# Kernel tuning notes

Hardware: AMD Instinct MI355X
Metric: run time of the kernel (lower is better)

Reference implementation:

```python
import jax, jax.numpy as jnp
import numpy as np

D_MODEL, D_INNER, D_STATE, D_CONV, DT_RANK = 2048, 4096, 16, 4, 128
B, T = 2, 1024


def setup_inputs() -> dict:
    key = jax.random.key(0)
    ks = jax.random.split(key, 8)
    dt_init_std = DT_RANK ** -0.5
    # dt bias init per the torch code: inv softplus of dt in [dt_min, dt_max]
    dt = jnp.exp(jax.random.uniform(ks[6], (D_INNER,)) * (np.log(0.1) - np.log(0.001)) + np.log(0.001))
    dt = jnp.clip(dt, 1e-4, None)
    dt_proj_b = dt + jnp.log(-jnp.expm1(-dt))
    A_log = jnp.log(jnp.tile(jnp.arange(1, D_STATE + 1, dtype=jnp.float32)[None, :], (D_INNER, 1)))
    return {
        "x": jax.random.normal(ks[0], (B, T, D_MODEL), jnp.float32),
        "h": jnp.zeros((B, D_INNER, D_STATE), jnp.float32),
        "conv_cache": jnp.zeros((B, D_INNER, D_CONV - 1), jnp.float32),
        "in_proj_w": jax.random.normal(ks[1], (2 * D_INNER, D_MODEL), jnp.float32) * 0.02,
        "conv_w": jax.random.normal(ks[2], (D_INNER, D_CONV), jnp.float32) * (1.0 / np.sqrt(D_CONV)),
        "conv_b": jnp.zeros((D_INNER,), jnp.float32),
        "x_proj_w": jax.random.normal(ks[3], (DT_RANK + 2 * D_STATE, D_INNER), jnp.float32) * 0.02,
        "dt_proj_w": jax.random.uniform(ks[4], (D_INNER, DT_RANK), jnp.float32, -dt_init_std, dt_init_std),
        "dt_proj_b": dt_proj_b,
        "A_log": A_log,
        "D_param": jnp.ones((D_INNER,), jnp.float32),
        "out_proj_w": jax.random.normal(ks[5], (D_MODEL, D_INNER), jnp.float32) * 0.02,
    }


def _forward(x, h, conv_cache, in_proj_w, conv_w, conv_b, x_proj_w,
             dt_proj_w, dt_proj_b, A_log, D_param, out_proj_w):
    Tlen = x.shape[1]
    xz = x @ in_proj_w.T                                  # (B,T,2*d_inner)
    xi, z = jnp.split(xz, 2, axis=-1)
    # causal depthwise conv with cache: concat history then valid conv
    xc = jnp.concatenate([jnp.swapaxes(conv_cache, 1, 2), xi], axis=1)  # (B,T+3,d_inner)
    new_conv_cache = jnp.swapaxes(xc[:, -(D_CONV - 1):, :], 1, 2)       # (B,d_inner,3)
    xconv = sum(xc[:, k:k + Tlen, :] * conv_w[:, k] for k in range(D_CONV)) + conv_b
    xs = jax.nn.silu(xconv)                               # (B,T,d_inner)
    # SSM params per step
    dbc = xs @ x_proj_w.T                                 # (B,T,dt_rank+2n)
    delta, Bm, Cm = jnp.split(dbc, [DT_RANK, DT_RANK + D_STATE], axis=-1)
    delta = jax.nn.softplus(delta @ dt_proj_w.T + dt_proj_b)  # (B,T,d_inner)
    A = -jnp.exp(A_log)                                   # (d_inner,n)
    dA = jnp.exp(jnp.einsum('btd,dn->btdn', delta, A))    # (B,T,d,n)
    dBx = jnp.einsum('btd,btn,btd->btdn', delta, Bm, xs)  # (B,T,d,n)

    def step(hc, inp):
        dA_t, dBx_t, C_t = inp
        hc = dA_t * hc + dBx_t                            # (B,d,n)
        return hc, jnp.einsum('bdn,bn->bd', hc, C_t)

    h_last, ys = jax.lax.scan(
        step, h,
        (jnp.moveaxis(dA, 1, 0), jnp.moveaxis(dBx, 1, 0), jnp.moveaxis(Cm, 1, 0)))
    y = jnp.moveaxis(ys, 0, 1) + D_param * xs             # (B,T,d_inner)
    out = (y * jax.nn.silu(z)) @ out_proj_w.T             # (B,T,d_model)
    return out, h_last, new_conv_cache


def reference(x, h, conv_cache, in_proj_w, conv_w, conv_b, x_proj_w,
              dt_proj_w, dt_proj_b, A_log, D_param, out_proj_w):
    return _forward(x, h, conv_cache, in_proj_w, conv_w, conv_b, x_proj_w,
                    dt_proj_w, dt_proj_b, A_log, D_param, out_proj_w)
```

## Files before the change

kernel.cpp:

```cpp
#include <hip/hip_runtime.h>
#include <hip/hip_bf16.h>
#include <math.h>

#define D_MODEL 2048
#define D_INNER 4096
#define D_STATE 16
#define D_CONV  4
#define DT_RANK 128
#define NB      2
#define TT      1024
#define M_TOT   (NB * TT)
#define NC      16
#define CL      64
#define TC      16

typedef __bf16 bf16x8_t __attribute__((ext_vector_type(8)));
typedef float  f32x4_t  __attribute__((ext_vector_type(4)));

__global__ __launch_bounds__(256) void fused_cast(
    const float* __restrict__ x,  const float* __restrict__ wi,
    const float* __restrict__ wo, const float* __restrict__ wx,
    const float* __restrict__ wdt,
    __bf16* __restrict__ x16,  __bf16* __restrict__ wi16,
    __bf16* __restrict__ wo16, __bf16* __restrict__ wx16,
    __bf16* __restrict__ wdt16, __bf16* __restrict__ dbc16)
{
    const size_t g = (size_t)blockIdx.x * 256 + threadIdx.x;
    const float* src; __bf16* dst; size_t off;
    if      (g < 524288)  { src = x;   dst = x16;   off = g; }
    else if (g < 2621440) { src = wi;  dst = wi16;  off = g - 524288; }
    else if (g < 3670016) { src = wo;  dst = wo16;  off = g - 2621440; }
    else if (g < 3801088) { off = g - 3670016; dst = wx16;
                            src = (g < 3751936) ? wx : nullptr; }
    else if (g < 3866624) { src = wdt; dst = wdt16; off = g - 3801088; }
    else                  { src = nullptr; dst = dbc16; off = g - 3866624; }

    bf16x8_t v;
    if (src) {
        const float4 f0 = ((const float4*)src)[2 * off];
        const float4 f1 = ((const float4*)src)[2 * off + 1];
        v[0] = (__bf16)f0.x; v[1] = (__bf16)f0.y; v[2] = (__bf16)f0.z; v[3] = (__bf16)f0.w;
        v[4] = (__bf16)f1.x; v[5] = (__bf16)f1.y; v[6] = (__bf16)f1.z; v[7] = (__bf16)f1.w;
    } else {
        v = (bf16x8_t)(__bf16)0.f;
    }
    ((bf16x8_t*)dst)[off] = v;
}

__global__ __launch_bounds__(256) void reduce_out(
    const float4* __restrict__ p0, const float4* __restrict__ p1,
    float4* __restrict__ o)
{
    const size_t g = (size_t)blockIdx.x * 256 + threadIdx.x;
    const float4 a = p0[g];
    const float4 b = p1[g];
    o[g] = make_float4(a.x + b.x, a.y + b.y, a.z + b.z, a.w + b.w);
}

__global__ __launch_bounds__(512, 2) void gemm_bf16_256(
    const __bf16* __restrict__ A, int lda,
    const __bf16* __restrict__ W, int ldw,
    __bf16* __restrict__ C, int ldc,
    int nt)
{
    __shared__ __bf16 As[4 * 128 * 64];
    __shared__ __bf16 Bs[4 * 128 * 64];

    const int tid = threadIdx.x;
    const int w   = tid >> 6;
    const int l   = tid & 63;
    const int m0  = blockIdx.y * 256;
    const int n0  = blockIdx.x * 256;
    const int wm  = (w >> 2) * 128;
    const int wn  = (w & 3) * 64;

    const int sl   = ((l & 7) ^ (l >> 3)) & 7;
    const int srow = 2 * (w * 16 + (l >> 3)) + (sl >> 2);
    const int scol = (sl & 3) * 8;
    const __bf16* gA = A + (size_t)(m0 + srow) * lda + scol;
    const __bf16* gB = W + (size_t)(n0 + srow) * ldw + scol;
    __bf16* lA = &As[(size_t)w * 1024];
    __bf16* lB = &Bs[(size_t)w * 1024];

    const int fr  = l & 15;
    const int swz = ((((fr & 1) * 4) + (l >> 4)) ^ ((fr >> 1) & 7)) * 8;
    const int aoff = wm * 32 + (fr >> 1) * 64 + swz;
    const int boff = wn * 32 + (fr >> 1) * 64 + swz;

    f32x4_t acc[8][4] = {};

#define STAGE_A(t, q) { \
    const __bf16* s0_ = gA + (size_t)(t) * 32; \
    __builtin_amdgcn_global_load_lds((const __attribute__((address_space(1))) void*)s0_, \
        (__attribute__((address_space(3))) void*)(lA + (q) * 8192), 16, 0, 0); \
    __builtin_amdgcn_global_load_lds((const __attribute__((address_space(1))) void*)(s0_ + (size_t)16 * lda), \
        (__attribute__((address_space(3))) void*)(lA + (q) * 8192 + 512), 16, 0, 0); }
#define STAGE_B(t, q) { \
    const __bf16* s0_ = gB + (size_t)(t) * 32; \
    __builtin_amdgcn_global_load_lds((const __attribute__((address_space(1))) void*)s0_, \
        (__attribute__((address_space(3))) void*)(lB + (q) * 8192), 16, 0, 0); \
    __builtin_amdgcn_global_load_lds((const __attribute__((address_space(1))) void*)(s0_ + (size_t)16 * ldw), \
        (__attribute__((address_space(3))) void*)(lB + (q) * 8192 + 512), 16, 0, 0); }

    STAGE_A(0, 0); STAGE_B(0, 0);
    STAGE_A(1, 1); STAGE_B(1, 1);
    asm volatile("s_waitcnt vmcnt(4)" ::: "memory");
    __builtin_amdgcn_s_barrier();

    for (int t = 0; t < nt; ++t) {
        const int q  = t & 3;
        const int qn = (t + 2) & 3;
        const __bf16* Aq = &As[q * 8192];
        const __bf16* Bq = &Bs[q * 8192];
        bf16x8_t av[4], bv[4];

#pragma unroll
        for (int i = 0; i < 4; i++)
            av[i] = *(const bf16x8_t*)&Aq[aoff + i * 512];
#pragma unroll
        for (int i = 0; i < 4; i++)
            bv[i] = *(const bf16x8_t*)&Bq[boff + i * 512];
        if (t + 2 < nt) STAGE_A(t + 2, qn);
        __builtin_amdgcn_s_barrier();
        asm volatile("s_waitcnt lgkmcnt(0)" ::: "memory");
        __builtin_amdgcn_sched_barrier(0);
        __builtin_amdgcn_s_setprio(1);
#pragma unroll
        for (int mt = 0; mt < 4; mt++)
#pragma unroll
            for (int nn = 0; nn < 4; nn++)
                acc[mt][nn] = __builtin_amdgcn_mfma_f32_16x16x32_bf16(
                    av[mt], bv[nn], acc[mt][nn], 0, 0, 0);
        __builtin_amdgcn_s_setprio(0);
        __builtin_amdgcn_s_barrier();

#pragma unroll
        for (int i = 0; i < 4; i++)
            av[i] = *(const bf16x8_t*)&Aq[aoff + (i + 4) * 512];
        if (t + 2 < nt) STAGE_B(t + 2, qn);
        __builtin_amdgcn_s_barrier();
        asm volatile("s_waitcnt lgkmcnt(0)" ::: "memory");
        __builtin_amdgcn_sched_barrier(0);
        __builtin_amdgcn_s_setprio(1);
#pragma unroll
        for (int mt = 0; mt < 4; mt++)
#pragma unroll
            for (int nn = 0; nn < 4; nn++)
                acc[mt + 4][nn] = __builtin_amdgcn_mfma_f32_16x16x32_bf16(
                    av[mt], bv[nn], acc[mt + 4][nn], 0, 0, 0);
        __builtin_amdgcn_s_setprio(0);
        if (t + 2 < nt) asm volatile("s_waitcnt vmcnt(4)" ::: "memory");
        else            asm volatile("s_waitcnt vmcnt(0)" ::: "memory");
        __builtin_amdgcn_s_barrier();
    }
#undef STAGE_A
#undef STAGE_B

    const int cn = n0 + wn + fr;
    const int rb = m0 + wm + (l >> 4) * 4;
#pragma unroll
    for (int mt = 0; mt < 8; mt++)
#pragma unroll
        for (int nn = 0; nn < 4; nn++)
#pragma unroll
            for (int r = 0; r < 4; r++)
                C[(size_t)(rb + mt * 16 + r) * ldc + cn + nn * 16] =
                    (__bf16)acc[mt][nn][r];
}

template <int EPI, int KSTEP, typename OutT>
__global__ __launch_bounds__(256) void gemm_bf16_nt(
    const __bf16* __restrict__ A, int lda,
    const __bf16* __restrict__ W, int ldw,
    OutT* __restrict__ C, int ldc,
    int Kloop, int Nmax, const float* __restrict__ bias, size_t czoff)
{
    __shared__ __bf16 As[128 * KSTEP];
    __shared__ __bf16 Bs[128 * KSTEP];

    const int tid  = threadIdx.x;
    const int wave = tid >> 6;
    const int lane = tid & 63;
    const int m0 = blockIdx.y * 128;
    const int n0 = blockIdx.x * 128;
    const int mw = (wave >> 1) * 64;
    const int nw = (wave & 1) * 64;
    const int koff = blockIdx.z * Kloop;
    C += (size_t)blockIdx.z * czoff;

    f32x4_t acc[4][4] = {};

    const int g0 = wave * 2;
    const int rA = g0 * 16 + (lane >> 2);
    const int kk = (lane & 3) * 8;

    const __bf16* gA0 = A + (size_t)(m0 + rA) * lda + kk + koff;
    const __bf16* gA1 = gA0 + (size_t)16 * lda;
    const __bf16* gB0 = W + (size_t)(n0 + rA) * ldw + kk + koff;
    const __bf16* gB1 = gB0 + (size_t)16 * ldw;

    __bf16* lA0 = &As[(size_t)g0 * 512];
    __bf16* lA1 = &As[(size_t)(g0 + 1) * 512];
    __bf16* lB0 = &Bs[(size_t)g0 * 512];
    __bf16* lB1 = &Bs[(size_t)(g0 + 1) * 512];

    const int fr = lane & 15;
    const int fk = (lane >> 4) * 8;

    for (int k0 = 0; k0 < Kloop; k0 += KSTEP) {
#pragma unroll
        for (int p = 0; p < KSTEP / 32; p++) {
            const int kp = k0 + p * 32;
            const int lp = p * 4096;
            __builtin_amdgcn_global_load_lds(
                (const __attribute__((address_space(1))) void*)(gA0 + kp),
                (__attribute__((address_space(3))) void*)(lA0 + lp), 16, 0, 0);
            __builtin_amdgcn_global_load_lds(
                (const __attribute__((address_space(1))) void*)(gA1 + kp),
                (__attribute__((address_space(3))) void*)(lA1 + lp), 16, 0, 0);
            __builtin_amdgcn_global_load_lds(
                (const __attribute__((address_space(1))) void*)(gB0 + kp),
                (__attribute__((address_space(3))) void*)(lB0 + lp), 16, 0, 0);
            __builtin_amdgcn_global_load_lds(
                (const __attribute__((address_space(1))) void*)(gB1 + kp),
                (__attribute__((address_space(3))) void*)(lB1 + lp), 16, 0, 0);
        }
        __syncthreads();

#pragma unroll
        for (int p = 0; p < KSTEP / 32; p++) {
            const int lp = p * 4096;
            bf16x8_t av[4], bv[4];
#pragma unroll
            for (int mt = 0; mt < 4; mt++)
                av[mt] = *(const bf16x8_t*)&As[lp + (mw + mt * 16 + fr) * 32 + fk];
#pragma unroll
            for (int nt = 0; nt < 4; nt++)
                bv[nt] = *(const bf16x8_t*)&Bs[lp + (nw + nt * 16 + fr) * 32 + fk];

#pragma unroll
            for (int mt = 0; mt < 4; mt++)
#pragma unroll
                for (int nt = 0; nt < 4; nt++)
                    acc[mt][nt] = __builtin_amdgcn_mfma_f32_16x16x32_bf16(
                        av[mt], bv[nt], acc[mt][nt], 0, 0, 0);
        }
        __syncthreads();
    }

    const int cn = n0 + nw + (lane & 15);
    const int rb = m0 + mw + (lane >> 4) * 4;
#pragma unroll
    for (int mt = 0; mt < 4; mt++)
#pragma unroll
        for (int nt = 0; nt < 4; nt++) {
            const int n = cn + nt * 16;
            if (n >= Nmax) continue;
#pragma unroll
            for (int r = 0; r < 4; r++) {
                float v = acc[mt][nt][r];
                OutT* p = &C[(size_t)(rb + mt * 16 + r) * ldc + n];
                if (EPI == 1) {
                    v += bias[n];
                    v = (v > 20.f) ? v : __logf(1.f + __expf(v));
                    *p = (OutT)v;
                } else if (EPI == 2) {
                    atomicAdd((float*)p, v);
                } else {
                    *p = (OutT)v;
                }
            }
        }
}

__global__ __launch_bounds__(256) void gemm_dt(
    const float* __restrict__ A,
    const __bf16* __restrict__ W,
    __bf16* __restrict__ C,
    const float* __restrict__ bias)
{
    __shared__ __bf16 As[4 * 64 * 32];
    __shared__ __bf16 Bs[4 * 64 * 32];

    const int tid  = threadIdx.x;
    const int wave = tid >> 6;
    const int lane = tid & 63;
    const int m0 = blockIdx.y * 64;
    const int n0 = blockIdx.x * 64;
    const int mw = (wave >> 1) * 32;
    const int nw = (wave & 1) * 32;

    {
        const int r  = tid >> 2;
        const int cg = (tid & 3) * 8;
        const float* gA = A + (size_t)(m0 + r) * 160 + cg;
#pragma unroll
        for (int p = 0; p < 4; p++) {
            const float4 f0 = *(const float4*)(gA + p * 32);
            const float4 f1 = *(const float4*)(gA + p * 32 + 4);
            bf16x8_t v;
            v[0] = (__bf16)f0.x; v[1] = (__bf16)f0.y; v[2] = (__bf16)f0.z; v[3] = (__bf16)f0.w;
            v[4] = (__bf16)f1.x; v[5] = (__bf16)f1.y; v[6] = (__bf16)f1.z; v[7] = (__bf16)f1.w;
            *(bf16x8_t*)&As[p * 2048 + r * 32 + cg] = v;
        }
    }
    {
        const int rB = wave * 16 + (lane >> 2);
        const int kk = (lane & 3) * 8;
        const __bf16* gB = W + (size_t)(n0 + rB) * 128 + kk;
        __bf16* lB = &Bs[wave * 512];
#pragma unroll
        for (int p = 0; p < 4; p++) {
            __builtin_amdgcn_global_load_lds(
                (const __attribute__((address_space(1))) void*)(gB + p * 32),
                (__attribute__((address_space(3))) void*)(lB + p * 2048), 16, 0, 0);
        }
    }
    __syncthreads();

    const int fr = lane & 15;
    const int fk = (lane >> 4) * 8;
    f32x4_t acc[2][2] = {};
#pragma unroll
    for (int p = 0; p < 4; p++) {
        bf16x8_t av[2], bv[2];
#pragma unroll
        for (int mt = 0; mt < 2; mt++)
            av[mt] = *(const bf16x8_t*)&As[p * 2048 + (mw + mt * 16 + fr) * 32 + fk];
#pragma unroll
        for (int nt = 0; nt < 2; nt++)
            bv[nt] = *(const bf16x8_t*)&Bs[p * 2048 + (nw + nt * 16 + fr) * 32 + fk];
#pragma unroll
        for (int mt = 0; mt < 2; mt++)
#pragma unroll
            for (int nt = 0; nt < 2; nt++)
                acc[mt][nt] = __builtin_amdgcn_mfma_f32_16x16x32_bf16(
                    av[mt], bv[nt], acc[mt][nt], 0, 0, 0);
    }

    const int cn = n0 + nw + (lane & 15);
    const int rb = m0 + mw + (lane >> 4) * 4;
#pragma unroll
    for (int mt = 0; mt < 2; mt++)
#pragma unroll
        for (int nt = 0; nt < 2; nt++) {
            const int n = cn + nt * 16;
            const float bs = bias[n];
#pragma unroll
            for (int r = 0; r < 4; r++) {
                float v = acc[mt][nt][r] + bs;
                v = (v > 20.f) ? v : __logf(1.f + __expf(v));
                C[(size_t)(rb + mt * 16 + r) * 4096 + n] = (__bf16)v;
            }
        }
}

__global__ __launch_bounds__(256) void conv_silu(
    const __bf16* __restrict__ xz16,
    const float* __restrict__ conv_cache,
    const float* __restrict__ conv_w,
    const float* __restrict__ conv_b,
    __bf16* __restrict__ xs16,
    float* __restrict__ cc_out)
{
    const int b  = blockIdx.z;
    const int d  = blockIdx.y * 256 + threadIdx.x;
    const int t0 = blockIdx.x * TC;

    const float4 w  = *(const float4*)&conv_w[d * 4];
    const float bias = conv_b[d];

    float v[TC + 3];
    if (t0 == 0) {
        v[0] = conv_cache[(b * D_INNER + d) * 3 + 0];
        v[1] = conv_cache[(b * D_INNER + d) * 3 + 1];
        v[2] = conv_cache[(b * D_INNER + d) * 3 + 2];
    } else {
        v[0] = (float)xz16[(size_t)(b * TT + t0 - 3) * 8192 + d];
        v[1] = (float)xz16[(size_t)(b * TT + t0 - 2) * 8192 + d];
        v[2] = (float)xz16[(size_t)(b * TT + t0 - 1) * 8192 + d];
    }
#pragma unroll
    for (int k = 0; k < TC; k++)
        v[k + 3] = (float)xz16[(size_t)(b * TT + t0 + k) * 8192 + d];

#pragma unroll
    for (int k = 0; k < TC; k++) {
        float c = v[k] * w.x + v[k + 1] * w.y + v[k + 2] * w.z + v[k + 3] * w.w + bias;
        float s = c / (1.f + __expf(-c));
        xs16[(size_t)(b * TT + t0 + k) * 4096 + d] = (__bf16)s;
    }

    if (t0 + TC == TT) {
        cc_out[(b * D_INNER + d) * 3 + 0] = v[TC];
        cc_out[(b * D_INNER + d) * 3 + 1] = v[TC + 1];
        cc_out[(b * D_INNER + d) * 3 + 2] = v[TC + 2];
    }
}

__global__ __launch_bounds__(256) void scan_phase_a(
    const __bf16* __restrict__ delta16,
    const float* __restrict__ dbc,
    const __bf16* __restrict__ xs16,
    const float* __restrict__ A_log,
    float* __restrict__ P,
    float* __restrict__ S)
{
    const int idx = blockIdx.x * 256 + threadIdx.x;
    const int sub = idx & 3;
    const int d   = (idx >> 2) & 4095;
    const int c   = (idx >> 14) & (NC - 1);
    const int b   = idx >> 18;

    const float4 Af = *(const float4*)&A_log[d * 16 + sub * 4];
    const float Ad0 = -__expf(Af.x), Ad1 = -__expf(Af.y);
    const float Ad2 = -__expf(Af.z), Ad3 = -__expf(Af.w);

    const int t0 = c * CL;
    const __bf16* pdelta = delta16 + (size_t)(b * TT + t0) * 4096 + d;
    const __bf16* px     = xs16 + (size_t)(b * TT + t0) * 4096 + d;
    const float*  pB     = dbc + ((size_t)b * TT + t0) * 160 + 128 + sub * 4;

    float h0 = 0.f, h1 = 0.f, h2 = 0.f, h3 = 0.f, sd = 0.f;
#pragma unroll 4
    for (int t = 0; t < CL; t++) {
        const float delta = (float)pdelta[(size_t)t * 4096];
        const float xv    = (float)px[(size_t)t * 4096];
        const float4 Bv   = *(const float4*)&pB[(size_t)t * 160];
        const float dx = delta * xv;
        h0 = __expf(delta * Ad0) * h0 + dx * Bv.x;
        h1 = __expf(delta * Ad1) * h1 + dx * Bv.y;
        h2 = __expf(delta * Ad2) * h2 + dx * Bv.z;
        h3 = __expf(delta * Ad3) * h3 + dx * Bv.w;
        sd += delta;
    }
    const size_t o = ((size_t)(b * NC + c) * 4096 + d) * 16 + sub * 4;
    *(float4*)&P[o] = make_float4(__expf(Ad0 * sd), __expf(Ad1 * sd),
                                  __expf(Ad2 * sd), __expf(Ad3 * sd));
    *(float4*)&S[o] = make_float4(h0, h1, h2, h3);
}

__global__ __launch_bounds__(256) void scan_phase_c(
    const __bf16* __restrict__ delta16,
    const __bf16* __restrict__ xz16,
    const float* __restrict__ dbc,
    const __bf16* __restrict__ xs16,
    const float* __restrict__ P,
    const float* __restrict__ S,
    const float* __restrict__ h_in,
    const float* __restrict__ A_log,
    const float* __restrict__ D_param,
    __bf16* __restrict__ ys16,
    float* __restrict__ h_out)
{
    const int idx = blockIdx.x * 256 + threadIdx.x;
    const int sub = idx & 3;
    const int d   = (idx >> 2) & 4095;
    const int c   = (idx >> 14) & (NC - 1);
    const int b   = idx >> 18;

    const float4 Af = *(const float4*)&A_log[d * 16 + sub * 4];
    const float Ad0 = -__expf(Af.x), Ad1 = -__expf(Af.y);
    const float Ad2 = -__expf(Af.z), Ad3 = -__expf(Af.w);
    const float Dp = D_param[d];

    float4 hf = *(const float4*)&h_in[((size_t)b * 4096 + d) * 16 + sub * 4];
    float h0 = hf.x, h1 = hf.y, h2 = hf.z, h3 = hf.w;
    for (int cc = 0; cc < c; cc++) {
        const size_t o2 = ((size_t)(b * NC + cc) * 4096 + d) * 16 + sub * 4;
        const float4 p = *(const float4*)&P[o2];
        const float4 s = *(const float4*)&S[o2];
        h0 = p.x * h0 + s.x;
        h1 = p.y * h1 + s.y;
        h2 = p.z * h2 + s.z;
        h3 = p.w * h3 + s.w;
    }

    const int t0 = c * CL;
    const __bf16* pdelta = delta16 + (size_t)(b * TT + t0) * 4096 + d;
    const __bf16* pz     = xz16 + (size_t)(b * TT + t0) * 8192 + 4096 + d;
    const __bf16* px     = xs16 + (size_t)(b * TT + t0) * 4096 + d;
    const float*  pB     = dbc + ((size_t)b * TT + t0) * 160 + 128 + sub * 4;
    const float*  pC     = pB + 16;
    __bf16* py = ys16 + (size_t)(b * TT + t0) * 4096 + d;

#pragma unroll 4
    for (int t = 0; t < CL; t++) {
        const float delta = (float)pdelta[(size_t)t * 4096];
        const float xv    = (float)px[(size_t)t * 4096];
        const float4 Bv   = *(const float4*)&pB[(size_t)t * 160];
        const float4 Cv   = *(const float4*)&pC[(size_t)t * 160];
        const float dx = delta * xv;

        h0 = __expf(delta * Ad0) * h0 + dx * Bv.x;
        h1 = __expf(delta * Ad1) * h1 + dx * Bv.y;
        h2 = __expf(delta * Ad2) * h2 + dx * Bv.z;
        h3 = __expf(delta * Ad3) * h3 + dx * Bv.w;

        float y = h0 * Cv.x + h1 * Cv.y + h2 * Cv.z + h3 * Cv.w;
        y += __shfl_xor(y, 1);
        y += __shfl_xor(y, 2);

        if (sub == 0) {
            const float zv = (float)pz[(size_t)t * 8192];
            y += Dp * xv;
            const float g = zv / (1.f + __expf(-zv));
            py[(size_t)t * 4096] = (__bf16)(y * g);
        }
    }

    if (c == NC - 1) {
        *(float4*)&h_out[((size_t)b * 4096 + d) * 16 + sub * 4] =
            make_float4(h0, h1, h2, h3);
    }
}

extern "C" void kernel_launch(void* const* d_in, const int* in_sizes, int n_in,
                              void* d_out, int out_size, void* d_ws, size_t ws_size,
                              hipStream_t stream)
{
    const float* x          = (const float*)d_in[0];
    const float* h_in       = (const float*)d_in[1];
    const float* conv_cache = (const float*)d_in[2];
    const float* in_proj_w  = (const float*)d_in[3];
    const float* conv_w     = (const float*)d_in[4];
    const float* conv_b     = (const float*)d_in[5];
    const float* x_proj_w   = (const float*)d_in[6];
    const float* dt_proj_w  = (const float*)d_in[7];
    const float* dt_proj_b  = (const float*)d_in[8];
    const float* A_log      = (const float*)d_in[9];
    const float* D_param    = (const float*)d_in[10];
    const float* out_proj_w = (const float*)d_in[11];

    float* out    = (float*)d_out;
    float* h_out  = (float*)d_out + (size_t)NB * TT * D_MODEL;
    float* cc_out = h_out + (size_t)NB * D_INNER * D_STATE;

    char* ws = (char*)d_ws;
    __bf16* xz16    = (__bf16*)(ws);
    float*  Pout    = (float*)(ws);
    __bf16* x16     = (__bf16*)(ws + 33554432);
    float*  Pbuf    = (float*)(ws + 33554432);
    __bf16* wi16    = (__bf16*)(ws + 41943040);
    __bf16* delta16 = (__bf16*)(ws + 41943040);
    float*  Sbuf    = (float*)(ws + 58720256);
    __bf16* wo16    = (__bf16*)(ws + 75497472);
    __bf16* xs16    = (__bf16*)(ws + 92274688);
    float*  dbc     = (float*)(ws + 109051904);
    __bf16* ys16    = (__bf16*)(ws + 110362624);
    __bf16* wx16    = (__bf16*)(ws + 127139840);
    __bf16* wdt16   = (__bf16*)(ws + 129236992);

    dim3 blk(256);

    fused_cast<<<dim3(15424), blk, 0, stream>>>(
        x, in_proj_w, out_proj_w, x_proj_w, dt_proj_w,
        x16, wi16, wo16, wx16, wdt16, (__bf16*)dbc);

    gemm_bf16_256<<<dim3(32, 8), dim3(512), 0, stream>>>(
        x16, 2048, wi16, 2048, xz16, 8192, 2048 / 32);

    conv_silu<<<dim3(TT / TC, D_INNER / 256, NB), blk, 0, stream>>>(
        xz16, conv_cache, conv_w, conv_b, xs16, cc_out);

    gemm_bf16_nt<2, 64, float><<<dim3(2, 16, 16), blk, 0, stream>>>(
        xs16, 4096, wx16, 4096, dbc, 160, 256, 160, nullptr, 0);

    gemm_dt<<<dim3(64, 32), blk, 0, stream>>>(dbc, wdt16, delta16, dt_proj_b);

    scan_phase_a<<<dim3(NB * D_INNER * NC * 4 / 256), blk, 0, stream>>>(
        delta16, dbc, xs16, A_log, Pbuf, Sbuf);
    scan_phase_c<<<dim3(NB * D_INNER * NC * 4 / 256), blk, 0, stream>>>(
        delta16, xz16, dbc, xs16, Pbuf, Sbuf, h_in, A_log, D_param, ys16, h_out);

    gemm_bf16_nt<0, 64, float><<<dim3(16, 16, 2), blk, 0, stream>>>(
        ys16, 4096, wo16, 4096, Pout, 2048, 2048, 2048, nullptr,
        (size_t)2048 * 2048);
    reduce_out<<<dim3(4096), blk, 0, stream>>>(
        (const float4*)Pout, (const float4*)(Pout + (size_t)2048 * 2048),
        (float4*)out);
}
```

Before: 425.3 us.

## Store delta, xs and z time-major per channel so scan reads contiguous vectors

The dt-projection epilogue and conv kernel now also write delta, xs and z in a transposed (batch, channel, time) layout, and both scan phases load eight consecutive timesteps with one 16-byte vector load per stream instead of strided scalar loads. The goal is to replace the scan's strided bf16 loads, each 8 KB apart, with contiguous vector reads. In exchange, conv_silu writes two extra transposed arrays, the gemm epilogue writes scattered 8-byte stores, and the workspace is rearranged to alias buffers differently. Within a wave the four sub lanes read the same address, and neighbouring d values now lie 2 KB apart, so coalescing across lanes gets worse.

```diff
diff --git a/kernel.cpp b/kernel.cpp
--- a/kernel.cpp
+++ b/kernel.cpp
@@ -15,6 +15,7 @@
 #define TC      16
 
 typedef __bf16 bf16x8_t __attribute__((ext_vector_type(8)));
+typedef __bf16 bf16x4_t __attribute__((ext_vector_type(4)));
 typedef float  f32x4_t  __attribute__((ext_vector_type(4)));
 
 __global__ __launch_bounds__(256) void fused_cast(
@@ -346,12 +347,17 @@
         for (int nt = 0; nt < 2; nt++) {
             const int n = cn + nt * 16;
             const float bs = bias[n];
+            bf16x4_t pk;
 #pragma unroll
             for (int r = 0; r < 4; r++) {
                 float v = acc[mt][nt][r] + bs;
                 v = (v > 20.f) ? v : __logf(1.f + __expf(v));
-                C[(size_t)(rb + mt * 16 + r) * 4096 + n] = (__bf16)v;
+                pk[r] = (__bf16)v;
             }
+            const int m  = rb + mt * 16;
+            const int bb = m >> 10;
+            const int tt = m & 1023;
+            *(bf16x4_t*)&C[((size_t)(bb * 4096 + n)) * 1024 + tt] = pk;
         }
 }
 
@@ -361,6 +367,8 @@
     const float* __restrict__ conv_w,
     const float* __restrict__ conv_b,
     __bf16* __restrict__ xs16,
+    __bf16* __restrict__ xsT,
+    __bf16* __restrict__ zT,
     float* __restrict__ cc_out)
 {
     const int b  = blockIdx.z;
@@ -384,12 +392,25 @@
     for (int k = 0; k < TC; k++)
         v[k + 3] = (float)xz16[(size_t)(b * TT + t0 + k) * 8192 + d];
 
+    bf16x8_t sv[2];
 #pragma unroll
     for (int k = 0; k < TC; k++) {
         float c = v[k] * w.x + v[k + 1] * w.y + v[k + 2] * w.z + v[k + 3] * w.w + bias;
         float s = c / (1.f + __expf(-c));
         xs16[(size_t)(b * TT + t0 + k) * 4096 + d] = (__bf16)s;
-    }
+        sv[k >> 3][k & 7] = (__bf16)s;
+    }
+
+    bf16x8_t zv[2];
+#pragma unroll
+    for (int k = 0; k < TC; k++)
+        zv[k >> 3][k & 7] = xz16[(size_t)(b * TT + t0 + k) * 8192 + 4096 + d];
+
+    const size_t to = ((size_t)(b * 4096 + d)) * 1024 + t0;
+    *(bf16x8_t*)&xsT[to]     = sv[0];
+    *(bf16x8_t*)&xsT[to + 8] = sv[1];
+    *(bf16x8_t*)&zT[to]      = zv[0];
+    *(bf16x8_t*)&zT[to + 8]  = zv[1];
 
     if (t0 + TC == TT) {
         cc_out[(b * D_INNER + d) * 3 + 0] = v[TC];
@@ -399,9 +420,9 @@
 }
 
 __global__ __launch_bounds__(256) void scan_phase_a(
-    const __bf16* __restrict__ delta16,
+    const __bf16* __restrict__ deltaT,
     const float* __restrict__ dbc,
-    const __bf16* __restrict__ xs16,
+    const __bf16* __restrict__ xsT,
     const float* __restrict__ A_log,
     float* __restrict__ P,
     float* __restrict__ S)
@@ -416,23 +437,27 @@
     const float Ad0 = -__expf(Af.x), Ad1 = -__expf(Af.y);
     const float Ad2 = -__expf(Af.z), Ad3 = -__expf(Af.w);
 
-    const int t0 = c * CL;
-    const __bf16* pdelta = delta16 + (size_t)(b * TT + t0) * 4096 + d;
-    const __bf16* px     = xs16 + (size_t)(b * TT + t0) * 4096 + d;
-    const float*  pB     = dbc + ((size_t)b * TT + t0) * 160 + 128 + sub * 4;
+    const size_t tb = ((size_t)(b * 4096 + d)) * 1024 + c * CL;
+    const __bf16* pdT = deltaT + tb;
+    const __bf16* pxT = xsT + tb;
+    const float*  pB  = dbc + ((size_t)b * TT + c * CL) * 160 + 128 + sub * 4;
 
     float h0 = 0.f, h1 = 0.f, h2 = 0.f, h3 = 0.f, sd = 0.f;
-#pragma unroll 4
-    for (int t = 0; t < CL; t++) {
-        const float delta = (float)pdelta[(size_t)t * 4096];
-        const float xv    = (float)px[(size_t)t * 4096];
-        const float4 Bv   = *(const float4*)&pB[(size_t)t * 160];
-        const float dx = delta * xv;
-        h0 = __expf(delta * Ad0) * h0 + dx * Bv.x;
-        h1 = __expf(delta * Ad1) * h1 + dx * Bv.y;
-        h2 = __expf(delta * Ad2) * h2 + dx * Bv.z;
-        h3 = __expf(delta * Ad3) * h3 + dx * Bv.w;
-        sd += delta;
+    for (int to = 0; to < CL; to += 8) {
+        const bf16x8_t dv = *(const bf16x8_t*)&pdT[to];
+        const bf16x8_t xv = *(const bf16x8_t*)&pxT[to];
+#pragma unroll
+        for (int k = 0; k < 8; k++) {
+            const float delta = (float)dv[k];
+            const float x     = (float)xv[k];
+            const float4 Bv   = *(const float4*)&pB[(size_t)(to + k) * 160];
+            const float dx = delta * x;
+            h0 = __expf(delta * Ad0) * h0 + dx * Bv.x;
+            h1 = __expf(delta * Ad1) * h1 + dx * Bv.y;
+            h2 = __expf(delta * Ad2) * h2 + dx * Bv.z;
+            h3 = __expf(delta * Ad3) * h3 + dx * Bv.w;
+            sd += delta;
+        }
     }
     const size_t o = ((size_t)(b * NC + c) * 4096 + d) * 16 + sub * 4;
     *(float4*)&P[o] = make_float4(__expf(Ad0 * sd), __expf(Ad1 * sd),
@@ -441,10 +466,10 @@
 }
 
 __global__ __launch_bounds__(256) void scan_phase_c(
-    const __bf16* __restrict__ delta16,
-    const __bf16* __restrict__ xz16,
+    const __bf16* __restrict__ deltaT,
+    const __bf16* __restrict__ zT,
     const float* __restrict__ dbc,
-    const __bf16* __restrict__ xs16,
+    const __bf16* __restrict__ xsT,
     const float* __restrict__ P,
     const float* __restrict__ S,
     const float* __restrict__ h_in,
@@ -476,36 +501,41 @@
         h3 = p.w * h3 + s.w;
     }
 
-    const int t0 = c * CL;
-    const __bf16* pdelta = delta16 + (size_t)(b * TT + t0) * 4096 + d;
-    const __bf16* pz     = xz16 + (size_t)(b * TT + t0) * 8192 + 4096 + d;
-    const __bf16* px     = xs16 + (size_t)(b * TT + t0) * 4096 + d;
-    const float*  pB     = dbc + ((size_t)b * TT + t0) * 160 + 128 + sub * 4;
-    const float*  pC     = pB + 16;
-    __bf16* py = ys16 + (size_t)(b * TT + t0) * 4096 + d;
-
-#pragma unroll 4
-    for (int t = 0; t < CL; t++) {
-        const float delta = (float)pdelta[(size_t)t * 4096];
-        const float xv    = (float)px[(size_t)t * 4096];
-        const float4 Bv   = *(const float4*)&pB[(size_t)t * 160];
-        const float4 Cv   = *(const float4*)&pC[(size_t)t * 160];
-        const float dx = delta * xv;
-
-        h0 = __expf(delta * Ad0) * h0 + dx * Bv.x;
-        h1 = __expf(delta * Ad1) * h1 + dx * Bv.y;
-        h2 = __expf(delta * Ad2) * h2 + dx * Bv.z;
-        h3 = __expf(delta * Ad3) * h3 + dx * Bv.w;
-
-        float y = h0 * Cv.x + h1 * Cv.y + h2 * Cv.z + h3 * Cv.w;
-        y += __shfl_xor(y, 1);
-        y += __shfl_xor(y, 2);
-
-        if (sub == 0) {
-            const float zv = (float)pz[(size_t)t * 8192];
-            y += Dp * xv;
-            const float g = zv / (1.f + __expf(-zv));
-            py[(size_t)t * 4096] = (__bf16)(y * g);
+    const size_t tb = ((size_t)(b * 4096 + d)) * 1024 + c * CL;
+    const __bf16* pdT = deltaT + tb;
+    const __bf16* pxT = xsT + tb;
+    const __bf16* pzT = zT + tb;
+    const float*  pB  = dbc + ((size_t)b * TT + c * CL) * 160 + 128 + sub * 4;
+    const float*  pC  = pB + 16;
+    __bf16* py = ys16 + ((size_t)b * TT + c * CL) * 4096 + d;
+
+    for (int to = 0; to < CL; to += 8) {
+        const bf16x8_t dv  = *(const bf16x8_t*)&pdT[to];
+        const bf16x8_t xv8 = *(const bf16x8_t*)&pxT[to];
+        const bf16x8_t zv8 = *(const bf16x8_t*)&pzT[to];
+#pragma unroll
+        for (int k = 0; k < 8; k++) {
+            const float delta = (float)dv[k];
+            const float x     = (float)xv8[k];
+            const float4 Bv   = *(const float4*)&pB[(size_t)(to + k) * 160];
+            const float4 Cv   = *(const float4*)&pC[(size_t)(to + k) * 160];
+            const float dx = delta * x;
+
+            h0 = __expf(delta * Ad0) * h0 + dx * Bv.x;
+            h1 = __expf(delta * Ad1) * h1 + dx * Bv.y;
+            h2 = __expf(delta * Ad2) * h2 + dx * Bv.z;
+            h3 = __expf(delta * Ad3) * h3 + dx * Bv.w;
+
+            float y = h0 * Cv.x + h1 * Cv.y + h2 * Cv.z + h3 * Cv.w;
+            y += __shfl_xor(y, 1);
+            y += __shfl_xor(y, 2);
+
+            if (sub == 0) {
+                const float zv = (float)zv8[k];
+                y += Dp * x;
+                const float g = zv / (1.f + __expf(-zv));
+                py[(size_t)(to + k) * 4096] = (__bf16)(y * g);
+            }
         }
     }
 
@@ -538,18 +568,20 @@
 
     char* ws = (char*)d_ws;
     __bf16* xz16    = (__bf16*)(ws);
+    float*  Pbuf    = (float*)(ws);
+    float*  Sbuf    = (float*)(ws + 8388608);
     float*  Pout    = (float*)(ws);
-    __bf16* x16     = (__bf16*)(ws + 33554432);
-    float*  Pbuf    = (float*)(ws + 33554432);
-    __bf16* wi16    = (__bf16*)(ws + 41943040);
-    __bf16* delta16 = (__bf16*)(ws + 41943040);
-    float*  Sbuf    = (float*)(ws + 58720256);
-    __bf16* wo16    = (__bf16*)(ws + 75497472);
-    __bf16* xs16    = (__bf16*)(ws + 92274688);
-    float*  dbc     = (float*)(ws + 109051904);
-    __bf16* ys16    = (__bf16*)(ws + 110362624);
-    __bf16* wx16    = (__bf16*)(ws + 127139840);
-    __bf16* wdt16   = (__bf16*)(ws + 129236992);
+    __bf16* wi16    = (__bf16*)(ws + 33554432);
+    __bf16* xsT     = (__bf16*)(ws + 33554432);
+    __bf16* zT      = (__bf16*)(ws + 50331648);
+    __bf16* x16     = (__bf16*)(ws + 67108864);
+    __bf16* deltaT  = (__bf16*)(ws + 67108864);
+    __bf16* wo16    = (__bf16*)(ws + 83886080);
+    __bf16* xs16    = (__bf16*)(ws + 100663296);
+    __bf16* ys16    = (__bf16*)(ws + 100663296);
+    __bf16* wx16    = (__bf16*)(ws + 117440512);
+    __bf16* wdt16   = (__bf16*)(ws + 119537664);
+    float*  dbc     = (float*)(ws + 120586240);
 
     dim3 blk(256);
 
@@ -561,17 +593,17 @@
         x16, 2048, wi16, 2048, xz16, 8192, 2048 / 32);
 
     conv_silu<<<dim3(TT / TC, D_INNER / 256, NB), blk, 0, stream>>>(
-        xz16, conv_cache, conv_w, conv_b, xs16, cc_out);
+        xz16, conv_cache, conv_w, conv_b, xs16, xsT, zT, cc_out);
 
     gemm_bf16_nt<2, 64, float><<<dim3(2, 16, 16), blk, 0, stream>>>(
         xs16, 4096, wx16, 4096, dbc, 160, 256, 160, nullptr, 0);
 
-    gemm_dt<<<dim3(64, 32), blk, 0, stream>>>(dbc, wdt16, delta16, dt_proj_b);
+    gemm_dt<<<dim3(64, 32), blk, 0, stream>>>(dbc, wdt16, deltaT, dt_proj_b);
 
     scan_phase_a<<<dim3(NB * D_INNER * NC * 4 / 256), blk, 0, stream>>>(
-        delta16, dbc, xs16, A_log, Pbuf, Sbuf);
+        deltaT, dbc, xsT, A_log, Pbuf, Sbuf);
     scan_phase_c<<<dim3(NB * D_INNER * NC * 4 / 256), blk, 0, stream>>>(
-        delta16, xz16, dbc, xs16, Pbuf, Sbuf, h_in, A_log, D_param, ys16, h_out);
+        deltaT, zT, dbc, xsT, Pbuf, Sbuf, h_in, A_log, D_param, ys16, h_out);
 
     gemm_bf16_nt<0, 64, float><<<dim3(16, 16, 2), blk, 0, stream>>>(
         ys16, 4096, wo16, 4096, Pout, 2048, 2048, 2048, nullptr,
```

After: 437.6 us. +2.9%, slower.
